# Kernel tuning notes

Measured on AMD Instinct MI355X. Metric: run time of the kernel, lower is better.

## Reference

```python
import jax, jax.numpy as jnp
import numpy as np

E = 4_194_304
N_COMPANY = 100_000
N_CAUSE, N_COURT, N_RES = 200, 50, 10
D_CA, D_COURT, D_CATE = 12, 4, 4
D = D_CA + D_COURT + D_CATE  # 20


def setup_inputs() -> dict:
    key = jax.random.key(0)
    ks = jax.random.split(key, 10)
    cause_idx = jax.random.randint(ks[0], (E,), 0, N_CAUSE, dtype=jnp.int32)
    court_idx = jax.random.randint(ks[1], (E,), 0, N_COURT, dtype=jnp.int32)
    cate_idx = jax.random.randint(ks[2], (E,), 0, N_RES, dtype=jnp.int32)
    seg_ids = jnp.sort(jax.random.randint(ks[3], (E,), 0, N_COMPANY, dtype=jnp.int32))
    time_interval = jax.random.uniform(ks[4], (E,), dtype=jnp.float32) * 365.0
    # learned parameters (nn.Embedding default init ~ N(0,1); Linear ~ U)
    ca_table = jax.random.normal(ks[5], (N_CAUSE, D_CA), dtype=jnp.float32)
    court_table = jax.random.normal(ks[6], (N_COURT, D_COURT), dtype=jnp.float32)
    cate_table = jax.random.normal(ks[7], (N_RES, D_CATE), dtype=jnp.float32)
    lim = 1.0 / np.sqrt(D)
    proj_w = jax.random.uniform(ks[8], (D, D), dtype=jnp.float32, minval=-lim, maxval=lim)
    decay_w = jax.random.uniform(ks[9], (), dtype=jnp.float32, minval=0.5, maxval=1.5)
    return {
        "cause_idx": cause_idx, "court_idx": court_idx, "cate_idx": cate_idx,
        "seg_ids": seg_ids, "time_interval": time_interval,
        "ca_table": ca_table, "court_table": court_table, "cate_table": cate_table,
        "proj_w": proj_w, "decay_w": decay_w,
    }


def reference(cause_idx, court_idx, cate_idx, seg_ids, time_interval,
              ca_table, court_table, cate_table, proj_w, decay_w):
    # per-event categorical embedding gather -> [E, 20]
    risk = jnp.concatenate(
        [ca_table[cause_idx], court_table[court_idx], cate_table[cate_idx]], axis=1)
    # Decayer: learnable scale times inverse-log time decay
    decay = decay_w / jnp.log(jnp.e + time_interval)  # [E]
    # proj(decay * risk): Linear(20, 20, bias=False) -> x @ W^T
    y = jnp.einsum('ed,od->eo', decay[:, None] * risk, proj_w)
    # per-company sum reduction (the original Python loop over companies)
    com_emb = jax.ops.segment_sum(y, seg_ids, num_segments=N_COMPANY,
                                  indices_are_sorted=True)
    return com_emb
```

## Files before the change

### kernel.cpp

```cpp
#include <hip/hip_runtime.h>

#define NCOMP   100000
#define D_CA    12
#define D_COURT 4
#define D_CATE  4
#define D_TOT   20
#define NCAUSE  200
#define NCOURT  50
#define NRES    10
#define CHUNK   16
#define TPB     256
#define BLK_EV  (TPB * CHUNK)
#define MAXSLOT 160

__device__ __forceinline__ void flush_run(const float (&acc)[D_TOT], int c, int c_first,
                                          float* __restrict__ lds_slot,
                                          const float* __restrict__ lds_w,
                                          float* __restrict__ out) {
    const int slot = c - c_first;
    if (slot < MAXSLOT) {
#pragma unroll
        for (int d = 0; d < D_TOT; ++d)
            atomicAdd(&lds_slot[slot * D_TOT + d], acc[d]);
    } else {
#pragma unroll 1
        for (int o = 0; o < D_TOT; ++o) {
            float s = 0.0f;
#pragma unroll 1
            for (int d = 0; d < D_TOT; ++d) s += acc[d] * lds_w[o * D_TOT + d];
            atomicAdd(&out[c * D_TOT + o], s);
        }
    }
}

__device__ __noinline__ void slow_chunk(long base, int jmax, float dw,
                                        const int* __restrict__ cause_idx,
                                        const int* __restrict__ court_idx,
                                        const int* __restrict__ cate_idx,
                                        const int* __restrict__ seg_ids,
                                        const float* __restrict__ time_interval,
                                        const float* lds_ca, const float* lds_court,
                                        const float* lds_cate, const float* lds_w,
                                        float* lds_slot, int c_first,
                                        float* __restrict__ out) {
    float acc[D_TOT];
#pragma unroll
    for (int d = 0; d < D_TOT; ++d) acc[d] = 0.0f;
    int cur = seg_ids[base];
#pragma unroll 1
    for (int j = 0; j < jmax; ++j) {
        const int sj = seg_ids[base + j];
        if (sj != cur) {
            flush_run(acc, cur, c_first, lds_slot, lds_w, out);
#pragma unroll
            for (int d = 0; d < D_TOT; ++d) acc[d] = 0.0f;
            cur = sj;
        }
        const int ca = cause_idx[base + j];
        const int co = court_idx[base + j];
        const int ct = cate_idx[base + j];
        const float t = time_interval[base + j];
        const float dec = __fdividef(dw, __logf(2.718281828459045f + t));
#pragma unroll 1
        for (int d = 0; d < D_CA; ++d) acc[d] += dec * lds_ca[ca * D_CA + d];
#pragma unroll 1
        for (int d = 0; d < D_COURT; ++d) acc[D_CA + d] += dec * lds_court[co * D_COURT + d];
#pragma unroll 1
        for (int d = 0; d < D_CATE; ++d) acc[D_CA + D_COURT + d] += dec * lds_cate[ct * D_CATE + d];
    }
    flush_run(acc, cur, c_first, lds_slot, lds_w, out);
}

__global__ __launch_bounds__(TPB)
void block_seg_kernel(const int* __restrict__ cause_idx,
                      const int* __restrict__ court_idx,
                      const int* __restrict__ cate_idx,
                      const int* __restrict__ seg_ids,
                      const float* __restrict__ time_interval,
                      const float* __restrict__ ca_table,
                      const float* __restrict__ court_table,
                      const float* __restrict__ cate_table,
                      const float* __restrict__ proj_w,
                      const float* __restrict__ decay_w,
                      int n_events,
                      float* __restrict__ out) {
    __shared__ __align__(16) float lds_ca[NCAUSE * D_CA];
    __shared__ __align__(16) float lds_court[NCOURT * D_COURT];
    __shared__ __align__(16) float lds_cate[NRES * D_CATE];
    __shared__ __align__(16) float lds_w[D_TOT * D_TOT];
    __shared__ __align__(16) float lds_slot[MAXSLOT * D_TOT];
    __shared__ int sh_c0, sh_c1;

    for (int i = threadIdx.x; i < NCAUSE * D_CA; i += TPB) lds_ca[i] = ca_table[i];
    for (int i = threadIdx.x; i < NCOURT * D_COURT; i += TPB) lds_court[i] = court_table[i];
    for (int i = threadIdx.x; i < NRES * D_CATE; i += TPB) lds_cate[i] = cate_table[i];
    for (int i = threadIdx.x; i < D_TOT * D_TOT; i += TPB) lds_w[i] = proj_w[i];
    for (int i = threadIdx.x; i < MAXSLOT * D_TOT; i += TPB) lds_slot[i] = 0.0f;
    if (threadIdx.x == 0) {
        const long b0 = (long)blockIdx.x * BLK_EV;
        long b1 = b0 + BLK_EV;
        if (b1 > n_events) b1 = n_events;
        sh_c0 = seg_ids[b0];
        sh_c1 = seg_ids[b1 - 1];
    }
    __syncthreads();

    const float dw = decay_w[0];
    const int c_first = sh_c0;
    const long base = (long)blockIdx.x * BLK_EV + (long)threadIdx.x * CHUNK;

    if (base < n_events) {
        if (base + CHUNK > n_events) {
            slow_chunk(base, (int)(n_events - base), dw, cause_idx, court_idx, cate_idx,
                       seg_ids, time_interval, lds_ca, lds_court, lds_cate, lds_w,
                       lds_slot, c_first, out);
        } else {
            const int4* seg4 = (const int4*)(seg_ids + base);
            const int4 s0 = seg4[0], s1 = seg4[1], s2 = seg4[2], s3 = seg4[3];
            const int first = s0.x, last = s3.w;

            const bool slow =
                ((s0.y != first) & (s0.y != last)) | ((s0.z != first) & (s0.z != last)) |
                ((s0.w != first) & (s0.w != last)) | ((s1.x != first) & (s1.x != last)) |
                ((s1.y != first) & (s1.y != last)) | ((s1.z != first) & (s1.z != last)) |
                ((s1.w != first) & (s1.w != last)) | ((s2.x != first) & (s2.x != last)) |
                ((s2.y != first) & (s2.y != last)) | ((s2.z != first) & (s2.z != last)) |
                ((s2.w != first) & (s2.w != last)) | ((s3.x != first) & (s3.x != last)) |
                ((s3.y != first) & (s3.y != last)) | ((s3.z != first) & (s3.z != last));

            if (slow) {
                slow_chunk(base, CHUNK, dw, cause_idx, court_idx, cate_idx,
                           seg_ids, time_interval, lds_ca, lds_court, lds_cate, lds_w,
                           lds_slot, c_first, out);
            } else {
                const int4* ca4 = (const int4*)(cause_idx + base);
                const int4* co4 = (const int4*)(court_idx + base);
                const int4* ct4 = (const int4*)(cate_idx + base);
                const float4* tm4 = (const float4*)(time_interval + base);

                float accH[D_TOT], accT[D_TOT];
#pragma unroll
                for (int d = 0; d < D_TOT; ++d) { accH[d] = 0.0f; accT[d] = 0.0f; }

#define PROC(CA, CO, CT, T, S)                                                \
    do {                                                                      \
        const float dec  = __fdividef(dw, __logf(2.718281828459045f + (T)));  \
        const float decT = ((S) != first) ? dec : 0.0f;                       \
        const float decH = dec - decT;                                        \
        const float4* car = (const float4*)(lds_ca + (CA) * D_CA);            \
        const float4 a0 = car[0], a1 = car[1], a2 = car[2];                   \
        const float4 b0 = *(const float4*)(lds_court + (CO) * D_COURT);       \
        const float4 c0 = *(const float4*)(lds_cate + (CT) * D_CATE);         \
        accH[0]  += decH * a0.x;  accT[0]  += decT * a0.x;                    \
        accH[1]  += decH * a0.y;  accT[1]  += decT * a0.y;                    \
        accH[2]  += decH * a0.z;  accT[2]  += decT * a0.z;                    \
        accH[3]  += decH * a0.w;  accT[3]  += decT * a0.w;                    \
        accH[4]  += decH * a1.x;  accT[4]  += decT * a1.x;                    \
        accH[5]  += decH * a1.y;  accT[5]  += decT * a1.y;                    \
        accH[6]  += decH * a1.z;  accT[6]  += decT * a1.z;                    \
        accH[7]  += decH * a1.w;  accT[7]  += decT * a1.w;                    \
        accH[8]  += decH * a2.x;  accT[8]  += decT * a2.x;                    \
        accH[9]  += decH * a2.y;  accT[9]  += decT * a2.y;                    \
        accH[10] += decH * a2.z;  accT[10] += decT * a2.z;                    \
        accH[11] += decH * a2.w;  accT[11] += decT * a2.w;                    \
        accH[12] += decH * b0.x;  accT[12] += decT * b0.x;                    \
        accH[13] += decH * b0.y;  accT[13] += decT * b0.y;                    \
        accH[14] += decH * b0.z;  accT[14] += decT * b0.z;                    \
        accH[15] += decH * b0.w;  accT[15] += decT * b0.w;                    \
        accH[16] += decH * c0.x;  accT[16] += decT * c0.x;                    \
        accH[17] += decH * c0.y;  accT[17] += decT * c0.y;                    \
        accH[18] += decH * c0.z;  accT[18] += decT * c0.z;                    \
        accH[19] += decH * c0.w;  accT[19] += decT * c0.w;                    \
    } while (0)

#define GROUP(J, SV)                                                          \
    do {                                                                      \
        const int4 ca = ca4[J]; const int4 co = co4[J];                       \
        const int4 ct = ct4[J]; const float4 tm = tm4[J];                     \
        PROC(ca.x, co.x, ct.x, tm.x, SV.x);                                   \
        PROC(ca.y, co.y, ct.y, tm.y, SV.y);                                   \
        PROC(ca.z, co.z, ct.z, tm.z, SV.z);                                   \
        PROC(ca.w, co.w, ct.w, tm.w, SV.w);                                   \
    } while (0)

                GROUP(0, s0);
                GROUP(1, s1);
                GROUP(2, s2);
                GROUP(3, s3);
#undef GROUP
#undef PROC

                flush_run(accH, first, c_first, lds_slot, lds_w, out);
                if (last != first)
                    flush_run(accT, last, c_first, lds_slot, lds_w, out);
            }
        }
    }

    __syncthreads();

    const int nslots = sh_c1 - c_first + 1;
    const int capped = nslots < MAXSLOT ? nslots : MAXSLOT;
    for (int i = threadIdx.x; i < capped * D_TOT; i += TPB) {
        const int slot = i / D_TOT;
        const int o = i - slot * D_TOT;
        float s = 0.0f;
#pragma unroll
        for (int d = 0; d < D_TOT; ++d) s += lds_slot[slot * D_TOT + d] * lds_w[o * D_TOT + d];
        const int c = c_first + slot;
        if (slot == 0 || slot == nslots - 1) atomicAdd(&out[c * D_TOT + o], s);
        else out[c * D_TOT + o] = s;
    }
}

extern "C" void kernel_launch(void* const* d_in, const int* in_sizes, int n_in,
                              void* d_out, int out_size, void* d_ws, size_t ws_size,
                              hipStream_t stream) {
    const int* cause_idx = (const int*)d_in[0];
    const int* court_idx = (const int*)d_in[1];
    const int* cate_idx  = (const int*)d_in[2];
    const int* seg_ids   = (const int*)d_in[3];
    const float* time_interval = (const float*)d_in[4];
    const float* ca_table      = (const float*)d_in[5];
    const float* court_table   = (const float*)d_in[6];
    const float* cate_table    = (const float*)d_in[7];
    const float* proj_w        = (const float*)d_in[8];
    const float* decay_w       = (const float*)d_in[9];
    float* out = (float*)d_out;
    const int n_events = in_sizes[0];

    hipMemsetAsync(out, 0, (size_t)out_size * sizeof(float), stream);

    const int blocks = (n_events + BLK_EV - 1) / BLK_EV;
    block_seg_kernel<<<blocks, TPB, 0, stream>>>(
        cause_idx, court_idx, cate_idx, seg_ids, time_interval,
        ca_table, court_table, cate_table, proj_w, decay_w,
        n_events, out);
}
```

Measured before the change: 184.9 us.

## Halve per-thread event chunk and hoist all index loads up front

Reduces events per thread from 16 to 8, doubling the grid and shrinking the per-block slot buffer, and adds a launch-bounds occupancy hint. All index, time and segment loads are issued at the top of the thread before compute, to expose memory-level parallelism. The head/tail split now uses a precomputed count of leading events in the first segment instead of per-event segment comparisons. This brings more blocks and more per-block flush atomics and reductions, plus register pressure from the occupancy hint.

```diff
diff --git a/kernel.cpp b/kernel.cpp
--- a/kernel.cpp
+++ b/kernel.cpp
@@ -8,10 +8,10 @@
 #define NCAUSE  200
 #define NCOURT  50
 #define NRES    10
-#define CHUNK   16
+#define CHUNK   8
 #define TPB     256
 #define BLK_EV  (TPB * CHUNK)
-#define MAXSLOT 160
+#define MAXSLOT 112
 
 __device__ __forceinline__ void flush_run(const float (&acc)[D_TOT], int c, int c_first,
                                           float* __restrict__ lds_slot,
@@ -71,7 +71,7 @@
     flush_run(acc, cur, c_first, lds_slot, lds_w, out);
 }
 
-__global__ __launch_bounds__(TPB)
+__global__ __launch_bounds__(TPB, 4)
 void block_seg_kernel(const int* __restrict__ cause_idx,
                       const int* __restrict__ court_idx,
                       const int* __restrict__ cate_idx,
@@ -115,37 +115,39 @@
                        seg_ids, time_interval, lds_ca, lds_court, lds_cate, lds_w,
                        lds_slot, c_first, out);
         } else {
-            const int4* seg4 = (const int4*)(seg_ids + base);
-            const int4 s0 = seg4[0], s1 = seg4[1], s2 = seg4[2], s3 = seg4[3];
-            const int first = s0.x, last = s3.w;
-
+            const int4   sa = ((const int4*)(seg_ids + base))[0];
+            const int4   sb = ((const int4*)(seg_ids + base))[1];
+            const int4   ca_a = ((const int4*)(cause_idx + base))[0];
+            const int4   ca_b = ((const int4*)(cause_idx + base))[1];
+            const int4   co_a = ((const int4*)(court_idx + base))[0];
+            const int4   co_b = ((const int4*)(court_idx + base))[1];
+            const int4   ct_a = ((const int4*)(cate_idx + base))[0];
+            const int4   ct_b = ((const int4*)(cate_idx + base))[1];
+            const float4 tm_a = ((const float4*)(time_interval + base))[0];
+            const float4 tm_b = ((const float4*)(time_interval + base))[1];
+
+            const int first = sa.x, last = sb.w;
             const bool slow =
-                ((s0.y != first) & (s0.y != last)) | ((s0.z != first) & (s0.z != last)) |
-                ((s0.w != first) & (s0.w != last)) | ((s1.x != first) & (s1.x != last)) |
-                ((s1.y != first) & (s1.y != last)) | ((s1.z != first) & (s1.z != last)) |
-                ((s1.w != first) & (s1.w != last)) | ((s2.x != first) & (s2.x != last)) |
-                ((s2.y != first) & (s2.y != last)) | ((s2.z != first) & (s2.z != last)) |
-                ((s2.w != first) & (s2.w != last)) | ((s3.x != first) & (s3.x != last)) |
-                ((s3.y != first) & (s3.y != last)) | ((s3.z != first) & (s3.z != last));
+                ((sa.y != first) & (sa.y != last)) | ((sa.z != first) & (sa.z != last)) |
+                ((sa.w != first) & (sa.w != last)) | ((sb.x != first) & (sb.x != last)) |
+                ((sb.y != first) & (sb.y != last)) | ((sb.z != first) & (sb.z != last));
+            const int k =
+                (sa.x == first) + (sa.y == first) + (sa.z == first) + (sa.w == first) +
+                (sb.x == first) + (sb.y == first) + (sb.z == first) + (sb.w == first);
 
             if (slow) {
                 slow_chunk(base, CHUNK, dw, cause_idx, court_idx, cate_idx,
                            seg_ids, time_interval, lds_ca, lds_court, lds_cate, lds_w,
                            lds_slot, c_first, out);
             } else {
-                const int4* ca4 = (const int4*)(cause_idx + base);
-                const int4* co4 = (const int4*)(court_idx + base);
-                const int4* ct4 = (const int4*)(cate_idx + base);
-                const float4* tm4 = (const float4*)(time_interval + base);
-
                 float accH[D_TOT], accT[D_TOT];
 #pragma unroll
                 for (int d = 0; d < D_TOT; ++d) { accH[d] = 0.0f; accT[d] = 0.0f; }
 
-#define PROC(CA, CO, CT, T, S)                                                \
+#define PROC(CA, CO, CT, T, E)                                                \
     do {                                                                      \
         const float dec  = __fdividef(dw, __logf(2.718281828459045f + (T)));  \
-        const float decT = ((S) != first) ? dec : 0.0f;                       \
+        const float decT = ((E) >= k) ? dec : 0.0f;                           \
         const float decH = dec - decT;                                        \
         const float4* car = (const float4*)(lds_ca + (CA) * D_CA);            \
         const float4 a0 = car[0], a1 = car[1], a2 = car[2];                   \
@@ -173,21 +175,14 @@
         accH[19] += decH * c0.w;  accT[19] += decT * c0.w;                    \
     } while (0)
 
-#define GROUP(J, SV)                                                          \
-    do {                                                                      \
-        const int4 ca = ca4[J]; const int4 co = co4[J];                       \
-        const int4 ct = ct4[J]; const float4 tm = tm4[J];                     \
-        PROC(ca.x, co.x, ct.x, tm.x, SV.x);                                   \
-        PROC(ca.y, co.y, ct.y, tm.y, SV.y);                                   \
-        PROC(ca.z, co.z, ct.z, tm.z, SV.z);                                   \
-        PROC(ca.w, co.w, ct.w, tm.w, SV.w);                                   \
-    } while (0)
-
-                GROUP(0, s0);
-                GROUP(1, s1);
-                GROUP(2, s2);
-                GROUP(3, s3);
-#undef GROUP
+                PROC(ca_a.x, co_a.x, ct_a.x, tm_a.x, 0);
+                PROC(ca_a.y, co_a.y, ct_a.y, tm_a.y, 1);
+                PROC(ca_a.z, co_a.z, ct_a.z, tm_a.z, 2);
+                PROC(ca_a.w, co_a.w, ct_a.w, tm_a.w, 3);
+                PROC(ca_b.x, co_b.x, ct_b.x, tm_b.x, 4);
+                PROC(ca_b.y, co_b.y, ct_b.y, tm_b.y, 5);
+                PROC(ca_b.z, co_b.z, ct_b.z, tm_b.z, 6);
+                PROC(ca_b.w, co_b.w, ct_b.w, tm_b.w, 7);
 #undef PROC
 
                 flush_run(accH, first, c_first, lds_slot, lds_w, out);
```

Result: slower. 232.9 us (+26.0%).
